# Kernel optimization log

Measured on AMD Instinct MI355X. Metric: run time of the kernel, lower is better.

Reference implementation:

```python
import jax, jax.numpy as jnp
import numpy as np

N_HEADS = 16
N_KV_HEADS = 4
N_EMBED = 2048
HEAD_DIM = 128
SECTIONS = [16, 24, 24, 16, 24, 24]


def _process_rotary(c):
    # c: [3, B, T, HEAD_DIM] -> [B, 1, T, HEAD_DIM]
    splits = np.cumsum(SECTIONS)[:-1]
    secs = jnp.split(c, splits, axis=-1)
    out = jnp.concatenate([s[i % 3] for i, s in enumerate(secs)], axis=-1)
    return out[:, None]  # add head axis


def _rotate_half(x):
    x1, x2 = jnp.split(x, 2, axis=-1)
    return jnp.concatenate([-x2, x1], axis=-1)


def setup_inputs() -> dict:
    key = jax.random.key(0)
    ks = jax.random.split(key, 12)
    B, T = 1, 2048
    s = 0.02
    return {
        "x": jax.random.normal(ks[0], (B, T, N_EMBED), jnp.float32),
        "cos": jax.random.uniform(ks[1], (3, B, T, HEAD_DIM), jnp.float32),
        "sin": jax.random.uniform(ks[2], (3, B, T, HEAD_DIM), jnp.float32),
        "Wq": jax.random.normal(ks[3], (N_EMBED, N_EMBED), jnp.float32) * s,
        "bq": jax.random.normal(ks[4], (N_EMBED,), jnp.float32) * s,
        "Wk": jax.random.normal(ks[5], (N_EMBED, N_KV_HEADS * HEAD_DIM), jnp.float32) * s,
        "bk": jax.random.normal(ks[6], (N_KV_HEADS * HEAD_DIM,), jnp.float32) * s,
        "Wv": jax.random.normal(ks[7], (N_EMBED, N_KV_HEADS * HEAD_DIM), jnp.float32) * s,
        "bv": jax.random.normal(ks[8], (N_KV_HEADS * HEAD_DIM,), jnp.float32) * s,
        "Wo": jax.random.normal(ks[9], (N_EMBED, N_EMBED), jnp.float32) * s,
    }


def reference(x, cos, sin, Wq, bq, Wk, bk, Wv, bv, Wo):
    B, T, C = x.shape
    H, Hkv, D = N_HEADS, N_KV_HEADS, HEAD_DIM
    q = (x @ Wq + bq).reshape(B, T, H, D).transpose(0, 2, 1, 3)    # [B,H,T,D]
    k = (x @ Wk + bk).reshape(B, T, Hkv, D).transpose(0, 2, 1, 3)  # [B,Hkv,T,D]
    v = (x @ Wv + bv).reshape(B, T, Hkv, D).transpose(0, 2, 1, 3)
    # multi-section rope (cos/sin are 4-dim -> custom path)
    c = _process_rotary(cos)
    s = _process_rotary(sin)
    q = q * c + _rotate_half(q) * s
    k = k * c + _rotate_half(k) * s
    present_k, present_v = k, v
    # GQA expansion (repeat_interleave over head axis)
    r = H // Hkv
    k = jnp.repeat(k, r, axis=1)
    v = jnp.repeat(v, r, axis=1)
    # causal SDPA
    scores = jnp.einsum("bhqd,bhkd->bhqk", q, k) / jnp.sqrt(jnp.float32(D))
    causal = jnp.tril(jnp.ones((T, T), dtype=bool))
    scores = jnp.where(causal, scores, jnp.finfo(scores.dtype).min)
    attn = jax.nn.softmax(scores, axis=-1)
    y = jnp.einsum("bhqk,bhkd->bhqd", attn, v)
    y = y.transpose(0, 2, 1, 3).reshape(B, T, C)
    y = y @ Wo
    return (y, present_k, present_v)
```

## Files before the change

kernel.cpp:

```cpp
#include <hip/hip_runtime.h>

typedef unsigned short u16;
typedef unsigned int u32;
typedef __attribute__((ext_vector_type(4))) float f32x4;
typedef __attribute__((ext_vector_type(8))) __bf16 bf16x8;
typedef __attribute__((ext_vector_type(4))) u16 u16x4;
typedef __attribute__((ext_vector_type(2))) u32 u32x2;


__device__ __forceinline__ u16 f2bf(float f) {
  union { float f; unsigned u; } v; v.f = f;
  unsigned r = v.u + 0x7fffu + ((v.u >> 16) & 1u);
  return (u16)(r >> 16);
}

__device__ __forceinline__ u32 pack_bf2(float a, float b) {
  union { float f; unsigned u; } x, y;
  x.f = a; y.f = b;
#if __has_builtin(__builtin_amdgcn_perm)
  return __builtin_amdgcn_perm(y.u + 0x8000u, x.u + 0x8000u, 0x07060302u);
#else
  return (u32)((x.u + 0x8000u) >> 16) | ((y.u + 0x8000u) & 0xffff0000u);
#endif
}

__device__ __forceinline__ void stage16(const void* g, void* l) {
#if __has_builtin(__builtin_amdgcn_global_load_lds)
  __builtin_amdgcn_global_load_lds((const __attribute__((address_space(1))) void*)g,
                                   (__attribute__((address_space(3))) void*)l, 16, 0, 0);
#else
  *(f32x4*)l = *(const f32x4*)g;
#endif
}

__device__ __forceinline__ f32x4 mfma16(bf16x8 a, bf16x8 b, f32x4 c) {
  return __builtin_amdgcn_mfma_f32_16x16x32_bf16(a, b, c, 0, 0, 0);
}

__device__ __forceinline__ float fexp2(float x) {
#if __has_builtin(__builtin_amdgcn_exp2f)
  return __builtin_amdgcn_exp2f(x);
#else
  return exp2f(x);
#endif
}

__device__ __forceinline__ int rope_ch(int d) {
  int dd = (d < 64) ? d : d - 64;
  return (dd < 16) ? 0 : (dd < 40 ? 1 : 2);
}


__global__ void yuna_prep(const float* __restrict__ x, u16* __restrict__ xb,
                          const float* __restrict__ cosp, const float* __restrict__ sinp,
                          float* __restrict__ csel, float* __restrict__ ssel,
                          const float* __restrict__ Wq, const float* __restrict__ Wk,
                          const float* __restrict__ Wv, const float* __restrict__ Wo,
                          u16* __restrict__ Wb, u16* __restrict__ Wob) {
  __shared__ float tile[64][65];
  const int bid = blockIdx.x;
  if (bid < 4096) {
    const int mat = bid >> 10;
    const int rem = bid & 1023;
    const float* W;
    u16* out;
    int N;
    if (mat == 0)      { W = Wq; out = Wb;                          N = 2048; }
    else if (mat == 1) { W = Wk; out = Wb + (size_t)2048 * 2048;    N = 512; }
    else if (mat == 2) { W = Wv; out = Wb + (size_t)2560 * 2048;    N = 512; }
    else               { W = Wo; out = Wob;                         N = 2048; }
    int k0 = (rem & 31) << 6, n0 = (rem >> 5) << 6;
    if (n0 >= N) return;
    int tx = threadIdx.x & 63, ty = threadIdx.x >> 6;
#pragma unroll
    for (int j = 0; j < 64; j += 4)
      tile[ty + j][tx] = W[(size_t)(k0 + ty + j) * N + n0 + tx];
    __syncthreads();
#pragma unroll
    for (int j = 0; j < 64; j += 4)
      out[(size_t)(n0 + ty + j) * 2048 + k0 + tx] = f2bf(tile[tx][ty + j]);
  } else if (bid < 8192) {
    int i = (bid - 4096) * 256 + threadIdx.x;
    f32x4 v = ((const f32x4*)x)[i];
    u16x4 o;
    o.x = f2bf(v.x); o.y = f2bf(v.y); o.z = f2bf(v.z); o.w = f2bf(v.w);
    ((u16x4*)xb)[i] = o;
  } else {
    int i = (bid - 8192) * 256 + threadIdx.x;
    int i4 = i * 4;
    int t = i4 >> 7, d = i4 & 127;
    f32x4 c, s;
#pragma unroll
    for (int j = 0; j < 4; ++j) {
      int ch = rope_ch(d + j);
      c[j] = cosp[(size_t)ch * 262144 + (size_t)t * 128 + d + j];
      s[j] = sinp[(size_t)ch * 262144 + (size_t)t * 128 + d + j];
    }
    ((f32x4*)csel)[i] = c;
    ((f32x4*)ssel)[i] = s;
  }
}

__global__ __launch_bounds__(256, 3) void yuna_gemm_qkv(
    const u16* __restrict__ A, const u16* __restrict__ Bt,
    const float* __restrict__ bq, const float* __restrict__ bk, const float* __restrict__ bv,
    const float* __restrict__ csel, const float* __restrict__ ssel,
    u16* __restrict__ qb, u16* __restrict__ kb, u16* __restrict__ vtb,
    float* __restrict__ pk, float* __restrict__ pv) {
  const int K = 2048;
  __shared__ __align__(16) char smem[49152];
  const int tid = threadIdx.x;
  const int wave = tid >> 6, lane = tid & 63;
  const int lrow = lane & 15, lkg = lane >> 4;
  const int m0 = blockIdx.x * 64;
  const int by = blockIdx.y;
  const int n0 = by * 128;
  const int sw = lrow & 7;

  const int srow = tid >> 3;
  const int ssc = (tid & 7) ^ ((tid >> 3) & 7);
  const size_t abase = (size_t)(m0 + srow) * K + ssc * 8;
  const size_t bbase = (size_t)(n0 + srow) * K + ssc * 8;

  const f32x4 fzero = {0.f, 0.f, 0.f, 0.f};
  f32x4 acc[4][2];
#pragma unroll
  for (int mi = 0; mi < 4; ++mi) { acc[mi][0] = fzero; acc[mi][1] = fzero; }

#pragma unroll
  for (int it = 0; it < 2; ++it)
    stage16(A + abase + (size_t)it * 32 * K, smem + (tid + it * 256) * 16);
#pragma unroll
  for (int it = 0; it < 4; ++it)
    stage16(Bt + bbase + (size_t)it * 32 * K, smem + 16384 + (tid + it * 256) * 16);

  for (int k0 = 0, ki = 0; k0 < K; k0 += 64, ++ki) {
    const int cur = ki & 1;
    const char* Asb = smem + cur * 8192;
    const char* Bsb = smem + 16384 + cur * 16384;
    if (k0 + 64 < K) {
      char* Asn = smem + (cur ^ 1) * 8192;
      char* Bsn = smem + 16384 + (cur ^ 1) * 16384;
#pragma unroll
      for (int it = 0; it < 2; ++it)
        stage16(A + abase + (size_t)it * 32 * K + k0 + 64, Asn + (tid + it * 256) * 16);
#pragma unroll
      for (int it = 0; it < 4; ++it)
        stage16(Bt + bbase + (size_t)it * 32 * K + k0 + 64, Bsn + (tid + it * 256) * 16);
      asm volatile("s_waitcnt vmcnt(6)\n\ts_barrier" ::: "memory");
    } else {
      asm volatile("s_waitcnt vmcnt(0)\n\ts_barrier" ::: "memory");
    }
#pragma unroll
    for (int kk = 0; kk < 2; ++kk) {
      const int cof = ((kk * 4 + lkg) ^ sw) << 4;
      bf16x8 af[4], bfr[2];
#pragma unroll
      for (int mi = 0; mi < 4; ++mi)
        af[mi] = *(const bf16x8*)(Asb + (mi * 16 + lrow) * 128 + cof);
#pragma unroll
      for (int ni = 0; ni < 2; ++ni)
        bfr[ni] = *(const bf16x8*)(Bsb + (wave * 16 + ni * 64 + lrow) * 128 + cof);
#pragma unroll
      for (int mi = 0; mi < 4; ++mi)
#pragma unroll
        for (int ni = 0; ni < 2; ++ni)
          acc[mi][ni] = mfma16(af[mi], bfr[ni], acc[mi][ni]);
    }
    asm volatile("s_barrier" ::: "memory");
  }

  if (by >= 20) {
    const int kvh = by - 20;
#pragma unroll
    for (int mi = 0; mi < 4; ++mi)
#pragma unroll
      for (int ni = 0; ni < 2; ++ni) {
        int d = wave * 16 + ni * 64 + lrow;
        float bb = bv[kvh * 128 + d];
        int mb = mi * 16 + lkg * 4;
        float v0 = acc[mi][ni][0] + bb, v1 = acc[mi][ni][1] + bb;
        float v2 = acc[mi][ni][2] + bb, v3 = acc[mi][ni][3] + bb;
        size_t pb = ((size_t)(kvh * 2048 + m0 + mb)) * 128 + d;
        pv[pb] = v0; pv[pb + 128] = v1; pv[pb + 256] = v2; pv[pb + 384] = v3;
        u16x4 w;
        w.x = f2bf(v0); w.y = f2bf(v1); w.z = f2bf(v2); w.w = f2bf(v3);
        *(u16x4*)(vtb + ((size_t)(kvh * 128 + d)) * 2048 + m0 + mb) = w;
      }
  } else {
    const float QSCALE = 1.4426950408889634f * 0.08838834764831845f;
    const bool isQ = (by < 16);
    const int h = isQ ? by : (by - 16);
    const float* bias = isQ ? bq : bk;
    const int dlo = wave * 16 + lrow;
    const float blo = bias[h * 128 + dlo];
    const float bhi = bias[h * 128 + dlo + 64];
#pragma unroll
    for (int mi = 0; mi < 4; ++mi) {
      const int tb = m0 + mi * 16 + lkg * 4;
#pragma unroll
      for (int r = 0; r < 4; ++r) {
        const int t = tb + r;
        float a = acc[mi][0][r] + blo;
        float b = acc[mi][1][r] + bhi;
        size_t cb = (size_t)t * 128 + dlo;
        float cl = csel[cb], sl = ssel[cb];
        float ch = csel[cb + 64], sh = ssel[cb + 64];
        float lo = a * cl - b * sl;
        float hi = b * ch + a * sh;
        size_t o = (((size_t)(h * 2048 + t)) << 7) + dlo;
        if (isQ) {
          qb[o] = f2bf(lo * QSCALE);
          qb[o + 64] = f2bf(hi * QSCALE);
        } else {
          kb[o] = f2bf(lo);
          kb[o + 64] = f2bf(hi);
          pk[o] = lo; pk[o + 64] = hi;
        }
      }
    }
  }
}

__global__ __launch_bounds__(256, 3) void yuna_gemm_out(
    const u16* __restrict__ A, const u16* __restrict__ Bt, float* __restrict__ C) {
  const int K = 2048;
  __shared__ __align__(16) char smem[49152];
  const int tid = threadIdx.x;
  const int wave = tid >> 6, lane = tid & 63;
  const int lrow = lane & 15, lkg = lane >> 4;
  const int m0 = blockIdx.x * 64;
  const int n0 = blockIdx.y * 128;
  const int wc = wave * 32;
  const int sw = lrow & 7;

  const int srow = tid >> 3;
  const int ssc = (tid & 7) ^ ((tid >> 3) & 7);
  const size_t abase = (size_t)(m0 + srow) * K + ssc * 8;
  const size_t bbase = (size_t)(n0 + srow) * K + ssc * 8;

  const f32x4 fzero = {0.f, 0.f, 0.f, 0.f};
  f32x4 acc[4][2];
#pragma unroll
  for (int mi = 0; mi < 4; ++mi) { acc[mi][0] = fzero; acc[mi][1] = fzero; }

#pragma unroll
  for (int it = 0; it < 2; ++it)
    stage16(A + abase + (size_t)it * 32 * K, smem + (tid + it * 256) * 16);
#pragma unroll
  for (int it = 0; it < 4; ++it)
    stage16(Bt + bbase + (size_t)it * 32 * K, smem + 16384 + (tid + it * 256) * 16);

  for (int k0 = 0, ki = 0; k0 < K; k0 += 64, ++ki) {
    const int cur = ki & 1;
    const char* Asb = smem + cur * 8192;
    const char* Bsb = smem + 16384 + cur * 16384;
    if (k0 + 64 < K) {
      char* Asn = smem + (cur ^ 1) * 8192;
      char* Bsn = smem + 16384 + (cur ^ 1) * 16384;
#pragma unroll
      for (int it = 0; it < 2; ++it)
        stage16(A + abase + (size_t)it * 32 * K + k0 + 64, Asn + (tid + it * 256) * 16);
#pragma unroll
      for (int it = 0; it < 4; ++it)
        stage16(Bt + bbase + (size_t)it * 32 * K + k0 + 64, Bsn + (tid + it * 256) * 16);
      asm volatile("s_waitcnt vmcnt(6)\n\ts_barrier" ::: "memory");
    } else {
      asm volatile("s_waitcnt vmcnt(0)\n\ts_barrier" ::: "memory");
    }
#pragma unroll
    for (int kk = 0; kk < 2; ++kk) {
      const int cof = ((kk * 4 + lkg) ^ sw) << 4;
      bf16x8 af[4], bfr[2];
#pragma unroll
      for (int mi = 0; mi < 4; ++mi)
        af[mi] = *(const bf16x8*)(Asb + (mi * 16 + lrow) * 128 + cof);
#pragma unroll
      for (int ni = 0; ni < 2; ++ni)
        bfr[ni] = *(const bf16x8*)(Bsb + (wc + ni * 16 + lrow) * 128 + cof);
#pragma unroll
      for (int mi = 0; mi < 4; ++mi)
#pragma unroll
        for (int ni = 0; ni < 2; ++ni)
          acc[mi][ni] = mfma16(af[mi], bfr[ni], acc[mi][ni]);
    }
    asm volatile("s_barrier" ::: "memory");
  }
#pragma unroll
  for (int mi = 0; mi < 4; ++mi)
#pragma unroll
    for (int ni = 0; ni < 2; ++ni) {
      int d = wc + ni * 16 + lrow;
      int mb = mi * 16 + lkg * 4;
#pragma unroll
      for (int r = 0; r < 4; ++r)
        C[(size_t)(m0 + mb + r) * 2048 + n0 + d] = acc[mi][ni][r];
    }
}

__global__ __launch_bounds__(512, 4) void yuna_flash_attn(
    const u16* __restrict__ Q,
    const u16* __restrict__ Kb,
    const u16* __restrict__ Vt,
    float* __restrict__ Op0,
    float* __restrict__ Op1,
    float* __restrict__ Op2,
    float* __restrict__ ml) {
  __shared__ __align__(16) u16 Ks[2][64 * 128];
  __shared__ __align__(16) u16 Vs[2][128 * 64];
  __shared__ __align__(16) u16 Ps[128 * 64];
  const int h = blockIdx.x;
  const int yb = blockIdx.y;
  const int qq = 15 - yb / 3;
  const int c = yb % 3;
  const int T = 2 * qq + 2;
  const int kb0 = c * T / 3;
  const int kb1 = (c + 1) * T / 3;
  const int kvh = h >> 2;
  const int tid = threadIdx.x, wave = tid >> 6, lane = tid & 63;
  const int lrow = lane & 15, lkg = lane >> 4;
  const int m = wave * 16 + lrow;
  const int sw = lrow & 7;
  const int qglob = qq * 128 + m;

  const int krow = tid >> 4;
  const int ksc = (tid & 15) ^ (krow & 7);
  const size_t kbase0 = ((size_t)(kvh * 2048 + krow) << 7) + ksc * 8;
  const int vrow = tid >> 3;
  const int vsc = (tid & 7) ^ (vrow & 7);
  const size_t vbase0 = (size_t)(kvh * 128 + vrow) * 2048 + vsc * 8;

  bf16x8 qf[4];
#pragma unroll
  for (int kk = 0; kk < 4; ++kk)
    qf[kk] = *(const bf16x8*)(Q + (((size_t)h * 2048 + qglob) << 7) + kk * 32 + lkg * 8);

  const f32x4 fzero = {0.f, 0.f, 0.f, 0.f};
  f32x4 o[8];
#pragma unroll
  for (int dt = 0; dt < 8; ++dt) o[dt] = fzero;
  float m_i = -1e30f, l_i = 0.f;

  if (kb0 < kb1) {
#pragma unroll
    for (int it = 0; it < 2; ++it)
      stage16(Kb + kbase0 + ((size_t)(kb0 * 64 + it * 32) << 7), (char*)Ks[0] + (tid + it * 512) * 16);
#pragma unroll
    for (int it = 0; it < 2; ++it)
      stage16(Vt + vbase0 + (size_t)it * 64 * 2048 + kb0 * 64, (char*)Vs[0] + (tid + it * 512) * 16);

    for (int kb = kb0; kb < kb1; ++kb) {
      const int cur = (kb - kb0) & 1;
      const char* Ksb = (const char*)Ks[cur];
      const char* Vsb = (const char*)Vs[cur];
      if (kb + 1 < kb1) {
        char* Ksn = (char*)Ks[cur ^ 1];
        char* Vsn = (char*)Vs[cur ^ 1];
#pragma unroll
        for (int it = 0; it < 2; ++it)
          stage16(Kb + kbase0 + ((size_t)((kb + 1) * 64 + it * 32) << 7), Ksn + (tid + it * 512) * 16);
#pragma unroll
        for (int it = 0; it < 2; ++it)
          stage16(Vt + vbase0 + (size_t)it * 64 * 2048 + (kb + 1) * 64, Vsn + (tid + it * 512) * 16);
        asm volatile("s_waitcnt vmcnt(4)\n\ts_barrier" ::: "memory");
      } else {
        asm volatile("s_waitcnt vmcnt(0)\n\ts_barrier" ::: "memory");
      }

      f32x4 s[4];
#pragma unroll
      for (int nt = 0; nt < 4; ++nt) s[nt] = fzero;
      __builtin_amdgcn_s_setprio(1);
#pragma unroll
      for (int kk = 0; kk < 4; ++kk) {
        const int cof = ((kk * 4 + lkg) ^ sw) << 4;
        bf16x8 kf[4];
#pragma unroll
        for (int nt = 0; nt < 4; ++nt)
          kf[nt] = *(const bf16x8*)(Ksb + (nt * 16 + lrow) * 256 + cof);
#pragma unroll
        for (int nt = 0; nt < 4; ++nt)
          s[nt] = mfma16(kf[nt], qf[kk], s[nt]);
      }
      __builtin_amdgcn_s_setprio(0);
      if (kb >= 2 * qq) {
        const int kbase = kb * 64 + lkg * 4;
#pragma unroll
        for (int nt = 0; nt < 4; ++nt)
#pragma unroll
          for (int r = 0; r < 4; ++r)
            if (kbase + nt * 16 + r > qglob) s[nt][r] = -3e38f;
      }

      float mxl = -1e30f;
#pragma unroll
      for (int nt = 0; nt < 4; ++nt)
#pragma unroll
        for (int r = 0; r < 4; ++r) mxl = fmaxf(mxl, s[nt][r]);
      if (__any(mxl > m_i + 8.0f)) {
        float mx = fmaxf(mxl, __shfl_xor(mxl, 16));
        mx = fmaxf(mx, __shfl_xor(mx, 32));
        float mnew = fmaxf(m_i, mx);
        float alpha = fexp2(m_i - mnew);
        m_i = mnew;
        l_i *= alpha;
#pragma unroll
        for (int dt = 0; dt < 8; ++dt) o[dt] *= alpha;
      }
      float ps = 0.f;
      const int hh = lkg & 1;
#pragma unroll
      for (int nt = 0; nt < 4; ++nt) {
        float p0 = fexp2(s[nt][0] - m_i);
        float p1 = fexp2(s[nt][1] - m_i);
        float p2 = fexp2(s[nt][2] - m_i);
        float p3 = fexp2(s[nt][3] - m_i);
        ps += (p0 + p1) + (p2 + p3);
        u32x2 pk2;
        pk2.x = pack_bf2(p0, p1);
        pk2.y = pack_bf2(p2, p3);
        int cc = 2 * nt + (lkg >> 1);
        *(u32x2*)((char*)Ps + m * 128 + ((cc ^ (m & 7)) << 4) + hh * 8) = pk2;
      }
      l_i += ps;

      __builtin_amdgcn_s_setprio(1);
#pragma unroll
      for (int kk = 0; kk < 2; ++kk) {
        const int cof = ((kk * 4 + lkg) ^ sw) << 4;
        bf16x8 pf = *(const bf16x8*)((char*)Ps + m * 128 + cof);
        bf16x8 vf[8];
#pragma unroll
        for (int dt = 0; dt < 8; ++dt)
          vf[dt] = *(const bf16x8*)(Vsb + (dt * 16 + lrow) * 128 + cof);
#pragma unroll
        for (int dt = 0; dt < 8; ++dt)
          o[dt] = mfma16(vf[dt], pf, o[dt]);
      }
      __builtin_amdgcn_s_setprio(0);
      asm volatile("s_barrier" ::: "memory");
    }
  }

  l_i += __shfl_xor(l_i, 16);
  l_i += __shfl_xor(l_i, 32);
  const size_t row = (size_t)h * 2048 + qglob;
  if (lkg == 0)
    *(float2*)(ml + ((size_t)(c * 32768) + row) * 2) = float2{m_i, l_i};
  float* Op = (c == 0) ? Op0 : (c == 1 ? Op1 : Op2);
  float* orow = Op + row * 128 + lkg * 4;
#pragma unroll
  for (int dt = 0; dt < 8; ++dt)
    *(f32x4*)(orow + dt * 16) = o[dt];
}

__global__ void yuna_merge(const float* __restrict__ Op0, const float* __restrict__ Op1,
                           const float* __restrict__ Op2, const float* __restrict__ ml,
                           u16* __restrict__ Y) {
  int idx = blockIdx.x * 256 + threadIdx.x;
  int d4 = idx & 31;
  int t = (idx >> 5) & 2047;
  int h = idx >> 16;
  size_t row = (size_t)h * 2048 + t;
  float2 a2 = *(const float2*)(ml + row * 2);
  float2 b2 = *(const float2*)(ml + (32768 + row) * 2);
  float2 c2 = *(const float2*)(ml + (65536 + row) * 2);
  float M = fmaxf(fmaxf(a2.x, b2.x), c2.x);
  float wA = fexp2(a2.x - M), wB = fexp2(b2.x - M), wC = fexp2(c2.x - M);
  float inv = 1.f / (a2.y * wA + b2.y * wB + c2.y * wC);
  wA *= inv; wB *= inv; wC *= inv;
  f32x4 a = ((const f32x4*)Op0)[row * 32 + d4];
  f32x4 b = ((const f32x4*)Op1)[row * 32 + d4];
  f32x4 cc = ((const f32x4*)Op2)[row * 32 + d4];
  u16x4 w;
  w.x = f2bf(a[0] * wA + b[0] * wB + cc[0] * wC);
  w.y = f2bf(a[1] * wA + b[1] * wB + cc[1] * wC);
  w.z = f2bf(a[2] * wA + b[2] * wB + cc[2] * wC);
  w.w = f2bf(a[3] * wA + b[3] * wB + cc[3] * wC);
  *(u16x4*)(Y + (size_t)t * 2048 + h * 128 + d4 * 4) = w;
}


extern "C" void kernel_launch(void* const* d_in, const int* in_sizes, int n_in,
                              void* d_out, int out_size, void* d_ws, size_t ws_size,
                              hipStream_t stream) {
  const float* x = (const float*)d_in[0];
  const float* cosp = (const float*)d_in[1];
  const float* sinp = (const float*)d_in[2];
  const float* Wq = (const float*)d_in[3];
  const float* bq = (const float*)d_in[4];
  const float* Wk = (const float*)d_in[5];
  const float* bk = (const float*)d_in[6];
  const float* Wv = (const float*)d_in[7];
  const float* bv = (const float*)d_in[8];
  const float* Wo = (const float*)d_in[9];
  float* out = (float*)d_out;
  float* out_k = out + 4194304;
  float* out_v = out + 5242880;

  char* ws = (char*)d_ws;
  u16* xb   = (u16*)(ws + 0);
  u16* Wb   = (u16*)(ws + 8388608);
  u16* Wob  = (u16*)(ws + 20971520);
  float* csel = (float*)(ws + 29360128);
  float* ssel = (float*)(ws + 30408704);
  u16* qbuf = (u16*)(ws + 54525952);
  u16* kbuf = (u16*)(ws + 62914560);
  u16* vtb  = (u16*)(ws + 65011712);
  u16* yat  = (u16*)(ws + 67108864);
  float* op0 = (float*)(ws + 0);
  float* mlb = (float*)(ws + 17825792);
  float* op1 = (float*)(ws + 31457280);
  float* op2 = (float*)(ws + 79691776);

  yuna_prep<<<8448, 256, 0, stream>>>(x, xb, cosp, sinp, csel, ssel,
                                      Wq, Wk, Wv, Wo, Wb, Wob);
  yuna_gemm_qkv<<<dim3(32, 24), 256, 0, stream>>>(xb, Wb, bq, bk, bv, csel, ssel,
                                                  qbuf, kbuf, vtb, out_k, out_v);
  yuna_flash_attn<<<dim3(16, 48), 512, 0, stream>>>(qbuf, kbuf, vtb, op0, op1, op2, mlb);
  yuna_merge<<<4096, 256, 0, stream>>>(op0, op1, op2, mlb, yat);
  yuna_gemm_out<<<dim3(32, 16), 256, 0, stream>>>(yat, Wob, out);
}
```

Before: 220.3 us.

## Shrink flash-attention blocks to 64 query rows and drop double buffering

The attention kernel now uses 256-thread blocks that each cover 64 query rows instead of 128, doubling the grid along the query axis. K/V staging in shared memory becomes single-buffered, and the next tile is loaded only after the current tile's compute and barrier. This cuts shared memory per block so more blocks can be resident per CU and makes causal work finer-grained. The cost is losing the overlap between global loads and compute within a block, and each K/V tile is reloaded by twice as many blocks.

```diff
diff --git a/kernel.cpp b/kernel.cpp
--- a/kernel.cpp
+++ b/kernel.cpp
@@ -298,7 +298,7 @@
     }
 }
 
-__global__ __launch_bounds__(512, 4) void yuna_flash_attn(
+__global__ __launch_bounds__(256, 4) void yuna_flash_attn(
     const u16* __restrict__ Q,
     const u16* __restrict__ Kb,
     const u16* __restrict__ Vt,
@@ -306,14 +306,14 @@
     float* __restrict__ Op1,
     float* __restrict__ Op2,
     float* __restrict__ ml) {
-  __shared__ __align__(16) u16 Ks[2][64 * 128];
-  __shared__ __align__(16) u16 Vs[2][128 * 64];
-  __shared__ __align__(16) u16 Ps[128 * 64];
+  __shared__ __align__(16) u16 Ks[64 * 128];
+  __shared__ __align__(16) u16 Vs[128 * 64];
+  __shared__ __align__(16) u16 Ps[64 * 64];
   const int h = blockIdx.x;
   const int yb = blockIdx.y;
-  const int qq = 15 - yb / 3;
+  const int qb = 31 - yb / 3;
   const int c = yb % 3;
-  const int T = 2 * qq + 2;
+  const int T = qb + 1;
   const int kb0 = c * T / 3;
   const int kb1 = (c + 1) * T / 3;
   const int kvh = h >> 2;
@@ -321,13 +321,13 @@
   const int lrow = lane & 15, lkg = lane >> 4;
   const int m = wave * 16 + lrow;
   const int sw = lrow & 7;
-  const int qglob = qq * 128 + m;
+  const int qglob = qb * 64 + m;
 
   const int krow = tid >> 4;
-  const int ksc = (tid & 15) ^ (krow & 7);
+  const int ksc = (tid & 15) ^ ((tid >> 4) & 7);
   const size_t kbase0 = ((size_t)(kvh * 2048 + krow) << 7) + ksc * 8;
   const int vrow = tid >> 3;
-  const int vsc = (tid & 7) ^ (vrow & 7);
+  const int vsc = (tid & 7) ^ ((tid >> 3) & 7);
   const size_t vbase0 = (size_t)(kvh * 128 + vrow) * 2048 + vsc * 8;
 
   bf16x8 qf[4];
@@ -343,29 +343,14 @@
 
   if (kb0 < kb1) {
 #pragma unroll
-    for (int it = 0; it < 2; ++it)
-      stage16(Kb + kbase0 + ((size_t)(kb0 * 64 + it * 32) << 7), (char*)Ks[0] + (tid + it * 512) * 16);
-#pragma unroll
-    for (int it = 0; it < 2; ++it)
-      stage16(Vt + vbase0 + (size_t)it * 64 * 2048 + kb0 * 64, (char*)Vs[0] + (tid + it * 512) * 16);
+    for (int it = 0; it < 4; ++it)
+      stage16(Kb + kbase0 + ((size_t)(kb0 * 64 + it * 16) << 7), (char*)Ks + (tid + it * 256) * 16);
+#pragma unroll
+    for (int it = 0; it < 4; ++it)
+      stage16(Vt + vbase0 + (size_t)it * 32 * 2048 + kb0 * 64, (char*)Vs + (tid + it * 256) * 16);
 
     for (int kb = kb0; kb < kb1; ++kb) {
-      const int cur = (kb - kb0) & 1;
-      const char* Ksb = (const char*)Ks[cur];
-      const char* Vsb = (const char*)Vs[cur];
-      if (kb + 1 < kb1) {
-        char* Ksn = (char*)Ks[cur ^ 1];
-        char* Vsn = (char*)Vs[cur ^ 1];
-#pragma unroll
-        for (int it = 0; it < 2; ++it)
-          stage16(Kb + kbase0 + ((size_t)((kb + 1) * 64 + it * 32) << 7), Ksn + (tid + it * 512) * 16);
-#pragma unroll
-        for (int it = 0; it < 2; ++it)
-          stage16(Vt + vbase0 + (size_t)it * 64 * 2048 + (kb + 1) * 64, Vsn + (tid + it * 512) * 16);
-        asm volatile("s_waitcnt vmcnt(4)\n\ts_barrier" ::: "memory");
-      } else {
-        asm volatile("s_waitcnt vmcnt(0)\n\ts_barrier" ::: "memory");
-      }
+      asm volatile("s_waitcnt vmcnt(0)\n\ts_barrier" ::: "memory");
 
       f32x4 s[4];
 #pragma unroll
@@ -377,19 +362,19 @@
         bf16x8 kf[4];
 #pragma unroll
         for (int nt = 0; nt < 4; ++nt)
-          kf[nt] = *(const bf16x8*)(Ksb + (nt * 16 + lrow) * 256 + cof);
+          kf[nt] = *(const bf16x8*)((const char*)Ks + (nt * 16 + lrow) * 256 + cof);
 #pragma unroll
         for (int nt = 0; nt < 4; ++nt)
           s[nt] = mfma16(kf[nt], qf[kk], s[nt]);
       }
       __builtin_amdgcn_s_setprio(0);
-      if (kb >= 2 * qq) {
+      if (kb == qb) {
         const int kbase = kb * 64 + lkg * 4;
 #pragma unroll
         for (int nt = 0; nt < 4; ++nt)
 #pragma unroll
           for (int r = 0; r < 4; ++r)
-            if (kbase + nt * 16 + r > qglob) s[nt][r] = -3e38f;
+            if (kbase + nt * 16 + r > qglob) s[nt][r] = -1e30f;
       }
 
       float mxl = -1e30f;
@@ -432,13 +417,21 @@
         bf16x8 vf[8];
 #pragma unroll
         for (int dt = 0; dt < 8; ++dt)
-          vf[dt] = *(const bf16x8*)(Vsb + (dt * 16 + lrow) * 128 + cof);
+          vf[dt] = *(const bf16x8*)((const char*)Vs + (dt * 16 + lrow) * 128 + cof);
 #pragma unroll
         for (int dt = 0; dt < 8; ++dt)
           o[dt] = mfma16(vf[dt], pf, o[dt]);
       }
       __builtin_amdgcn_s_setprio(0);
       asm volatile("s_barrier" ::: "memory");
+      if (kb + 1 < kb1) {
+#pragma unroll
+        for (int it = 0; it < 4; ++it)
+          stage16(Kb + kbase0 + ((size_t)((kb + 1) * 64 + it * 16) << 7), (char*)Ks + (tid + it * 256) * 16);
+#pragma unroll
+        for (int it = 0; it < 4; ++it)
+          stage16(Vt + vbase0 + (size_t)it * 32 * 2048 + (kb + 1) * 64, (char*)Vs + (tid + it * 256) * 16);
+      }
     }
   }
 
@@ -517,7 +510,7 @@
                                       Wq, Wk, Wv, Wo, Wb, Wob);
   yuna_gemm_qkv<<<dim3(32, 24), 256, 0, stream>>>(xb, Wb, bq, bk, bv, csel, ssel,
                                                   qbuf, kbuf, vtb, out_k, out_v);
-  yuna_flash_attn<<<dim3(16, 48), 512, 0, stream>>>(qbuf, kbuf, vtb, op0, op1, op2, mlb);
+  yuna_flash_attn<<<dim3(16, 96), 256, 0, stream>>>(qbuf, kbuf, vtb, op0, op1, op2, mlb);
   yuna_merge<<<4096, 256, 0, stream>>>(op0, op1, op2, mlb, yat);
   yuna_gemm_out<<<dim3(32, 16), 256, 0, stream>>>(yat, Wob, out);
 }
```

New measurement: 221.9 us. No clear change (+0.7%).
